# Optimization experiments

Measured on AMD Instinct MI355X. Metric: run time of the kernel, lower is better.

The kernel has to match this reference:

```python
import jax, jax.numpy as jnp
import numpy as np

B, T, H, PRED = 16384, 8, 256, 12


def _cell(x, h, c, Wih, Whh, bih, bhh):
    # PyTorch LSTM gate order: i, f, g, o
    g = x @ Wih.T + h @ Whh.T + bih + bhh
    i, f, gg, o = jnp.split(g, 4, axis=-1)
    c = jax.nn.sigmoid(f) * c + jax.nn.sigmoid(i) * jnp.tanh(gg)
    h = jax.nn.sigmoid(o) * jnp.tanh(c)
    return h, c


def _run_seq(x, layers):
    # stacked LSTM over full sequence, zero initial state; x: [B, T, D]
    b = x.shape[0]
    inp = x
    hs, cs = [], []
    for (Wih, Whh, bih, bhh) in layers:
        h0 = jnp.zeros((b, Whh.shape[1]), x.dtype)

        def step(carry, xt, Wih=Wih, Whh=Whh, bih=bih, bhh=bhh):
            h, c = _cell(xt, carry[0], carry[1], Wih, Whh, bih, bhh)
            return (h, c), h

        (h, c), out = jax.lax.scan(step, (h0, h0), jnp.swapaxes(inp, 0, 1))
        inp = jnp.swapaxes(out, 0, 1)
        hs.append(h)
        cs.append(c)
    return inp, jnp.stack(hs), jnp.stack(cs)


def _step_stack(x, hs, cs, layers):
    # single-timestep pass through stacked LSTM; hs/cs: [L, B, H]
    inp = x
    nh, nc = [], []
    for l, (Wih, Whh, bih, bhh) in enumerate(layers):
        h, c = _cell(inp, hs[l], cs[l], Wih, Whh, bih, bhh)
        inp = h
        nh.append(h)
        nc.append(c)
    return inp, jnp.stack(nh), jnp.stack(nc)


def _forward(x, l1_Wih0, l1_Whh0, l1_bih0, l1_bhh0, l1_Wih1, l1_Whh1, l1_bih1, l1_bhh1,
             l2_Wih0, l2_Whh0, l2_bih0, l2_bhh0, l2_Wih1, l2_Whh1, l2_bih1, l2_bhh1,
             fc1_w, fc1_b, fc2_w, fc2_b):
    L1 = [(l1_Wih0, l1_Whh0, l1_bih0, l1_bhh0), (l1_Wih1, l1_Whh1, l1_bih1, l1_bhh1)]
    L2 = [(l2_Wih0, l2_Whh0, l2_bih0, l2_bhh0), (l2_Wih1, l2_Whh1, l2_bih1, l2_bhh1)]
    out1, h1, c1 = _run_seq(x, L1)           # encode observed track
    _, h2, c2 = _run_seq(out1, L2)
    pos = x[:, -1, :]

    def dec(carry, _):
        pos, h1, c1, h2, c2 = carry
        o1, h1, c1 = _step_stack(pos, h1, c1, L1)
        o2, h2, c2 = _step_stack(o1, h2, c2, L2)
        delta = jax.nn.relu(o2 @ fc1_w.T + fc1_b) @ fc2_w.T + fc2_b
        pos = pos + delta
        return (pos, h1, c1, h2, c2), pos

    _, preds = jax.lax.scan(dec, (pos, h1, c1, h2, c2), None, length=PRED)
    return jnp.swapaxes(preds, 0, 1)  # [B, PRED, 2]


def setup_inputs() -> dict:
    key = jax.random.key(0)
    ks = iter(jax.random.split(key, 32))
    s = 1.0 / np.sqrt(H)  # matches PyTorch LSTM/Linear init scale

    def mk(shape):
        return jax.random.uniform(next(ks), shape, jnp.float32, -s, s)

    d = {"x": jax.random.normal(next(ks), (B, T, 2), jnp.float32)}
    for name, in_dim in [("l1", 2), ("l2", H)]:
        for layer in range(2):
            di = in_dim if layer == 0 else H
            d[f"{name}_Wih{layer}"] = mk((4 * H, di))
            d[f"{name}_Whh{layer}"] = mk((4 * H, H))
            d[f"{name}_bih{layer}"] = mk((4 * H,))
            d[f"{name}_bhh{layer}"] = mk((4 * H,))
    d["fc1_w"] = mk((H, H))
    d["fc1_b"] = mk((H,))
    d["fc2_w"] = mk((2, H))
    d["fc2_b"] = mk((2,))
    return d


def reference(x, l1_Wih0, l1_Whh0, l1_bih0, l1_bhh0, l1_Wih1, l1_Whh1, l1_bih1, l1_bhh1,
              l2_Wih0, l2_Whh0, l2_bih0, l2_bhh0, l2_Wih1, l2_Whh1, l2_bih1, l2_bhh1,
              fc1_w, fc1_b, fc2_w, fc2_b):
    return _forward(x, l1_Wih0, l1_Whh0, l1_bih0, l1_bhh0, l1_Wih1, l1_Whh1, l1_bih1, l1_bhh1,
                    l2_Wih0, l2_Whh0, l2_bih0, l2_bhh0, l2_Wih1, l2_Whh1, l2_bih1, l2_bhh1,
                    fc1_w, fc1_b, fc2_w, fc2_b)
```

## Files before the change

kernel.cpp:

```cpp
#include <hip/hip_runtime.h>
#include <hip/hip_cooperative_groups.h>
#include <stdint.h>

namespace cg = cooperative_groups;

#define Bsz   16384
#define Tseq  8
#define NPRED 12

typedef __attribute__((ext_vector_type(4))) float    f32x4;
typedef _Float16 h16;
typedef __attribute__((ext_vector_type(8))) _Float16 h16x8;

__device__ __forceinline__ float sigf(float x)   { return 1.f / (1.f + __expf(-x)); }
__device__ __forceinline__ float tanh_f(float x) { return 1.f - 2.f / (__expf(2.f * x) + 1.f); }

__device__ __forceinline__ void gload_lds16(const void* g, void* l) {
  __builtin_amdgcn_global_load_lds(
      (const __attribute__((address_space(1))) void*)g,
      (__attribute__((address_space(3))) void*)l, 16, 0, 0);
}

__global__ void mark_r12(float* __restrict__ out) {
  if (blockIdx.x == 0 && threadIdx.x < 64) out[threadIdx.x] = 1000.0f;
}
__global__ void seed_r12(float* __restrict__ pos, const float* __restrict__ x) {
  int b = blockIdx.x * 256 + threadIdx.x;
  pos[2 * b]     = x[(size_t)b * 16 + 14];
  pos[2 * b + 1] = x[(size_t)b * 16 + 15];
}

__global__ void pack_w(h16* __restrict__ dst, const float* __restrict__ W0,
                       const float* __restrict__ W1, int ksplit, int Kw, int Np,
                       int gatePack) {
  int idx = blockIdx.x * 256 + threadIdx.x;
  if (idx >= Np * Kw) return;
  int np = idx / Kw, k = idx - np * Kw;
  int n = np;
  if (gatePack) {
    int jb = np >> 7, wc = (np >> 6) & 1, gi = (np >> 4) & 3, jr = np & 15;
    n = gi * 256 + jb * 32 + wc * 16 + jr;
  }
  float w = (k < ksplit) ? W0[(size_t)n * ksplit + k]
                         : W1[(size_t)n * (Kw - ksplit) + (k - ksplit)];
  int KB = Kw >> 6;
  int jb = np >> 7, r = np & 127, kb = k >> 6;
  uint32_t byte = (uint32_t)(jb * KB + kb) * 16384u + (uint32_t)r * 128u
                + ((2u * (uint32_t)(k & 63)) ^ (uint32_t)((r & 7) << 4));
  *(h16*)((char*)dst + byte) = (h16)w;
}

__global__ void add_bias(float* __restrict__ dst, const float* __restrict__ a,
                         const float* __restrict__ b) {
  int i = blockIdx.x * 256 + threadIdx.x;
  if (i < 1024) dst[i] = a[i] + b[i];
}

__global__ void l0t0_pw(const float* __restrict__ x, const float* __restrict__ wih0,
                        const float* __restrict__ bias, h16* __restrict__ Cst,
                        char* __restrict__ hout) {
  int gid = blockIdx.x * 256 + threadIdx.x;
  int b = gid >> 5, jb = (gid & 31) << 3;
  float x0 = x[(size_t)b * 16], x1 = x[(size_t)b * 16 + 1];
  h16 cc[8]; h16 hh[8];
#pragma unroll
  for (int q = 0; q < 8; ++q) {
    int j = jb + q;
    float vi = bias[j]       + x0 * wih0[2 * j]           + x1 * wih0[2 * j + 1];
    float vg = bias[512 + j] + x0 * wih0[2 * (512 + j)]   + x1 * wih0[2 * (512 + j) + 1];
    float vo = bias[768 + j] + x0 * wih0[2 * (768 + j)]   + x1 * wih0[2 * (768 + j) + 1];
    float cn = sigf(vi) * tanh_f(vg);
    hh[q] = (h16)(sigf(vo) * tanh_f(cn));
    cc[q] = (h16)cn;
  }
  *(h16x8*)(Cst + (size_t)b * 256 + jb) = *(h16x8*)cc;
  *(h16x8*)(hout + (size_t)b * 512 + (((unsigned)jb * 2) ^ (unsigned)((b & 7) << 4))) = *(h16x8*)hh;
}

__device__ __forceinline__ void gemm_core(
    const char* A0, const char* A1, const char* Wp, int KB, int by, int m0,
    char* ldsA, char* ldsB, int tid, f32x4 acc[4][4]) {
  const int wave = tid >> 6, lane = tid & 63;
  const int rowa = tid >> 3;
  const int chb  = (tid & 7) * 16;

#pragma unroll
  for (int m = 0; m < 4; m++)
#pragma unroll
    for (int n = 0; n < 4; n++)
#pragma unroll
      for (int e = 0; e < 4; e++) acc[m][n][e] = 0.f;

  const char* aCur   = A0 + (size_t)(m0 + rowa) * 512 + chb;
  const char* a1Base = A1 + (size_t)(m0 + rowa) * 512 + chb;
  const char* wCur   = Wp + (size_t)by * KB * 16384 + rowa * 128 + chb;

  const int wr = wave >> 1, wc = wave & 1;

  for (int kb = 0; kb < KB; ++kb) {
    if (kb == 4) aCur = a1Base;
#pragma unroll
    for (int it = 0; it < 4; ++it) {
      gload_lds16(aCur + it * 16384, ldsA + it * 4096 + wave * 1024);
      gload_lds16(wCur + it * 4096,  ldsB + it * 4096 + wave * 1024);
    }
    __syncthreads();
#pragma unroll
    for (int kk = 0; kk < 2; ++kk) {
      const int kbyte = kk * 64 + (lane >> 4) * 16;
      h16x8 af[4], bfr[4];
#pragma unroll
      for (int mt = 0; mt < 4; ++mt) {
        int r = wr * 64 + mt * 16 + (lane & 15);
        af[mt] = *(const h16x8*)(ldsA + r * 128 + (kbyte ^ ((r & 7) << 4)));
      }
#pragma unroll
      for (int nt = 0; nt < 4; ++nt) {
        int c = wc * 64 + nt * 16 + (lane & 15);
        bfr[nt] = *(const h16x8*)(ldsB + c * 128 + (kbyte ^ ((c & 7) << 4)));
      }
#pragma unroll
      for (int mt = 0; mt < 4; ++mt)
#pragma unroll
        for (int nt = 0; nt < 4; ++nt)
          acc[mt][nt] = __builtin_amdgcn_mfma_f32_16x16x32_f16(af[mt], bfr[nt], acc[mt][nt], 0, 0, 0);
    }
    __syncthreads();
    aCur += 128;
    wCur += 16384;
  }
}

__device__ __forceinline__ void lstm_epilogue(
    f32x4 acc[4][4], int m0, int n0, int tid, const float* bias,
    const float* wih0, const float* xbase, int xstride, int hasx, int skipc,
    h16* Cst, char* hout) {
  const int wave = tid >> 6, lane = tid & 63;
  const int wr = wave >> 1, wc = wave & 1;
  const int j = (n0 >> 2) + wc * 16 + (lane & 15);
  const float bi = bias[j], bff = bias[256 + j], bg = bias[512 + j], bo = bias[768 + j];
  float wi0 = 0, wi1 = 0, wf0 = 0, wf1 = 0, wg0 = 0, wg1 = 0, wo0 = 0, wo1 = 0;
  if (hasx) {
    wi0 = wih0[2 * j];           wi1 = wih0[2 * j + 1];
    wf0 = wih0[2 * (256 + j)];   wf1 = wih0[2 * (256 + j) + 1];
    wg0 = wih0[2 * (512 + j)];   wg1 = wih0[2 * (512 + j) + 1];
    wo0 = wih0[2 * (768 + j)];   wo1 = wih0[2 * (768 + j) + 1];
  }
#pragma unroll
  for (int mt = 0; mt < 4; ++mt) {
#pragma unroll
    for (int e = 0; e < 4; e++) {
      const int b = m0 + wr * 64 + mt * 16 + (lane >> 4) * 4 + e;
      float vi = acc[mt][0][e] + bi;
      float vf = acc[mt][1][e] + bff;
      float vg = acc[mt][2][e] + bg;
      float vo = acc[mt][3][e] + bo;
      if (hasx) {
        const float x0 = xbase[(size_t)b * xstride];
        const float x1 = xbase[(size_t)b * xstride + 1];
        vi += x0 * wi0 + x1 * wi1;
        vf += x0 * wf0 + x1 * wf1;
        vg += x0 * wg0 + x1 * wg1;
        vo += x0 * wo0 + x1 * wo1;
      }
      const size_t ci = (size_t)b * 256 + j;
      float cn = sigf(vi) * tanh_f(vg);
      if (!skipc) cn += sigf(vf) * (float)Cst[ci];
      float h = sigf(vo) * tanh_f(cn);
      Cst[ci] = (h16)cn;
      *(h16*)(hout + (size_t)b * 512 + (((unsigned)j * 2) ^ (unsigned)((b & 7) << 4))) = (h16)h;
    }
  }
}

__device__ __forceinline__ void head_body(
    const char* A, const char* Wp, const float* b1, const float* w2,
    const float* b2, float* pos, float* out, int s, int blk, int tid, char* lds) {
  const int m0 = blk * 128;
  const int wave = tid >> 6, lane = tid & 63;
  const int wr = wave >> 1, wc = wave & 1;
  const int bl2 = tid >> 1, comp = tid & 1;

  float a = 0.f;
  for (int half = 0; half < 2; ++half) {
    f32x4 acc[4][4];
    gemm_core(A, A, Wp, 4, half, m0, lds, lds + 16384, tid, acc);
    h16* strip = (h16*)lds;
#pragma unroll
    for (int nt = 0; nt < 4; ++nt) {
      const int n = half * 128 + wc * 64 + nt * 16 + (lane & 15);
      const int nl = wc * 64 + nt * 16 + (lane & 15);
      const float bn = b1[n];
#pragma unroll
      for (int mt = 0; mt < 4; ++mt)
#pragma unroll
        for (int e = 0; e < 4; e++) {
          const int bl = wr * 64 + mt * 16 + (lane >> 4) * 4 + e;
          float v = acc[mt][nt][e] + bn;
          strip[bl * 134 + nl] = (h16)(v > 0.f ? v : 0.f);
        }
    }
    __syncthreads();
    const float* wrow = w2 + comp * 256 + half * 128;
#pragma unroll 8
    for (int n = 0; n < 128; ++n)
      a += (float)strip[bl2 * 134 + n] * wrow[n];
    __syncthreads();
  }
  const size_t b = (size_t)(m0 + bl2);
  float p = pos[2 * b + comp] + a + b2[comp];
  pos[2 * b + comp] = p;
  out[b * (NPRED * 2) + s * 2 + comp] = p;
}

struct CellDesc {
  const char* A0; const char* A1; const char* Wp;
  const float* bias; const float* wih0; const float* xbase;
  h16* Cst; char* hout;
  int Kw; int xstride; int hasx; int skipc;
};
struct Fused4 { CellDesc c[4]; };

__global__ __launch_bounds__(256, 4) void cells_diag(Fused4 args) {
  const int cellid = blockIdx.x >> 10;
  const int lid    = blockIdx.x & 1023;
  const CellDesc d = args.c[cellid];

  __shared__ __align__(16) char lds[32768];
  const int tid = threadIdx.x;

  int swz = (lid & 7) * 128 + (lid >> 3);
  const int by = swz & 7, bx = swz >> 3;
  const int m0 = bx * 128, n0 = by * 128;

  f32x4 acc[4][4];
  gemm_core(d.A0, d.A1, d.Wp, d.Kw >> 6, by, m0, lds, lds + 16384, tid, acc);
  lstm_epilogue(acc, m0, n0, tid, d.bias, d.wih0, d.xbase, d.xstride, d.hasx,
                d.skipc, d.Cst, d.hout);
}

struct DecArgs {
  char* hb0[2]; char* hb1[2]; char* hb2[2]; char* hb3[2];
  h16* Cs0; h16* Cs1; h16* Cs2; h16* Cs3;
  const char* wp10; const char* wp0; const char* wp1; const char* wp2; const char* wpf1;
  const float* biasc; const float* wih0;
  const float* fc1_b; const float* fc2_w; const float* fc2_b;
  float* pos; float* out;
};

__global__ __launch_bounds__(256, 4) void decoder_coop(DecArgs a) {
  cg::grid_group grid = cg::this_grid();
  __shared__ __align__(16) char lds[34304];
  const int tid = threadIdx.x;
  const int lid = blockIdx.x;
  int swz = (lid & 7) * 128 + (lid >> 3);
  const int by = swz & 7, bx = swz >> 3;
  const int m0 = bx * 128, n0 = by * 128;

  for (int s = 0; s < NPRED; ++s) {
    const int u = Tseq + s, cur = u & 1, prev = cur ^ 1;
    {
      f32x4 acc[4][4];
      gemm_core(a.hb0[prev], a.hb0[prev], a.wp10, 4, by, m0, lds, lds + 16384, tid, acc);
      lstm_epilogue(acc, m0, n0, tid, a.biasc, a.wih0, a.pos, 2, 1, 0, a.Cs0, a.hb0[cur]);
    }
    __threadfence();  grid.sync();
    {
      f32x4 acc[4][4];
      gemm_core(a.hb0[cur], a.hb1[prev], a.wp0, 8, by, m0, lds, lds + 16384, tid, acc);
      lstm_epilogue(acc, m0, n0, tid, a.biasc + 1024, nullptr, nullptr, 0, 0, 0, a.Cs1, a.hb1[cur]);
    }
    __threadfence();  grid.sync();
    {
      f32x4 acc[4][4];
      gemm_core(a.hb1[cur], a.hb2[prev], a.wp1, 8, by, m0, lds, lds + 16384, tid, acc);
      lstm_epilogue(acc, m0, n0, tid, a.biasc + 2048, nullptr, nullptr, 0, 0, 0, a.Cs2, a.hb2[cur]);
    }
    __threadfence();  grid.sync();
    {
      f32x4 acc[4][4];
      gemm_core(a.hb2[cur], a.hb3[prev], a.wp2, 8, by, m0, lds, lds + 16384, tid, acc);
      lstm_epilogue(acc, m0, n0, tid, a.biasc + 3072, nullptr, nullptr, 0, 0, 0, a.Cs3, a.hb3[cur]);
    }
    __threadfence();  grid.sync();
    if (lid < 128)
      head_body(a.hb3[cur], a.wpf1, a.fc1_b, a.fc2_w, a.fc2_b, a.pos, a.out, s, lid, tid, lds);
    __threadfence();  grid.sync();
  }
}

template <int NSEG, int HASX>
__global__ __launch_bounds__(256, 4) void cell_gemm(
    const char* __restrict__ A0, const char* __restrict__ A1,
    const char* __restrict__ Wp, int Kw,
    const float* __restrict__ bias, const float* __restrict__ wih0,
    const float* __restrict__ xbase, int xstride,
    h16* __restrict__ Cst, char* __restrict__ hout) {
  __shared__ __align__(16) char lds[32768];
  const int tid = threadIdx.x;
  int lid = blockIdx.x;
  int chunkv = gridDim.x >> 3;
  int swz = (lid & 7) * chunkv + (lid >> 3);
  const int by = swz % 8, bx = swz / 8;
  const int m0 = bx * 128, n0 = by * 128;
  f32x4 acc[4][4];
  gemm_core(A0, NSEG == 2 ? A1 : A0, Wp, Kw >> 6, by, m0, lds, lds + 16384, tid, acc);
  lstm_epilogue(acc, m0, n0, tid, bias, wih0, xbase, xstride, HASX, 0, Cst, hout);
}

__global__ __launch_bounds__(256) void fc_head(
    const char* __restrict__ A, const char* __restrict__ Wp,
    const float* __restrict__ b1, const float* __restrict__ w2,
    const float* __restrict__ b2, float* __restrict__ pos,
    float* __restrict__ out, int s) {
  __shared__ __align__(16) char lds[34304];
  head_body(A, Wp, b1, w2, b2, pos, out, s, blockIdx.x, threadIdx.x, lds);
}

extern "C" void kernel_launch(void* const* d_in, const int* in_sizes, int n_in,
                              void* d_out, int out_size, void* d_ws, size_t ws_size,
                              hipStream_t stream) {
  const float* x      = (const float*)d_in[0];
  const float* Wih[4] = {(const float*)d_in[1], (const float*)d_in[5],
                         (const float*)d_in[9], (const float*)d_in[13]};
  const float* Whh[4] = {(const float*)d_in[2], (const float*)d_in[6],
                         (const float*)d_in[10], (const float*)d_in[14]};
  const float* bih[4] = {(const float*)d_in[3], (const float*)d_in[7],
                         (const float*)d_in[11], (const float*)d_in[15]};
  const float* bhh[4] = {(const float*)d_in[4], (const float*)d_in[8],
                         (const float*)d_in[12], (const float*)d_in[16]};
  const float* fc1_w = (const float*)d_in[17];
  const float* fc1_b = (const float*)d_in[18];
  const float* fc2_w = (const float*)d_in[19];
  const float* fc2_b = (const float*)d_in[20];

  char* ws = (char*)d_ws;
  size_t off = 0;
  auto alloc = [&](size_t bytes) -> char* {
    char* p = ws + off;
    off += (bytes + 255) & ~(size_t)255;
    return p;
  };

  h16* Cs[4];
  for (int l = 0; l < 4; l++) Cs[l] = (h16*)alloc((size_t)Bsz * 256 * 2);
  char* h10[2] = {alloc((size_t)Bsz * 512), alloc((size_t)Bsz * 512)};
  char* sl[2]  = {alloc((size_t)Bsz * 512), alloc((size_t)Bsz * 512)};
  char* h20[2] = {alloc((size_t)Bsz * 512), alloc((size_t)Bsz * 512)};
  char* h21[2] = {alloc((size_t)Bsz * 512), alloc((size_t)Bsz * 512)};
  float* pos = (float*)alloc((size_t)Bsz * 2 * 4);
  float* biasc = (float*)alloc(4 * 1024 * 4);
  h16* wp10 = (h16*)alloc((size_t)1024 * 256 * 2);
  h16* wp[3];
  for (int i = 0; i < 3; i++) wp[i] = (h16*)alloc((size_t)1024 * 512 * 2);
  h16* wpf1 = (h16*)alloc((size_t)256 * 256 * 2);

  if (ws_size < off) {
    mark_r12<<<dim3(1), dim3(64), 0, stream>>>((float*)d_out);
    return;
  }

  seed_r12<<<dim3(Bsz / 256), dim3(256), 0, stream>>>(pos, x);

  pack_w<<<dim3((1024 * 256 + 255) / 256), dim3(256), 0, stream>>>(wp10, Whh[0], Whh[0], 256, 256, 1024, 1);
  pack_w<<<dim3((1024 * 512 + 255) / 256), dim3(256), 0, stream>>>(wp[0], Wih[1], Whh[1], 256, 512, 1024, 1);
  pack_w<<<dim3((1024 * 512 + 255) / 256), dim3(256), 0, stream>>>(wp[1], Wih[2], Whh[2], 256, 512, 1024, 1);
  pack_w<<<dim3((1024 * 512 + 255) / 256), dim3(256), 0, stream>>>(wp[2], Wih[3], Whh[3], 256, 512, 1024, 1);
  pack_w<<<dim3((256 * 256 + 255) / 256), dim3(256), 0, stream>>>(wpf1, fc1_w, fc1_w, 256, 256, 256, 0);
  for (int l = 0; l < 4; l++)
    add_bias<<<dim3(4), dim3(256), 0, stream>>>(biasc + l * 1024, bih[l], bhh[l]);

  char* hbuf[4][2] = {{h10[0], h10[1]}, {sl[0], sl[1]}, {h20[0], h20[1]}, {h21[0], h21[1]}};
  const h16* wpl[4] = {wp10, wp[0], wp[1], wp[2]};
  for (int d = 0; d <= 10; d++) {
    if (d == 0) {
      l0t0_pw<<<dim3(2048), dim3(256), 0, stream>>>(x, Wih[0], biasc, Cs[0], hbuf[0][0]);
      continue;
    }
    Fused4 args;
    int nc = 0;
    for (int l = 0; l < 4; l++) {
      int t = d - l;
      if (t < 0 || t >= Tseq) continue;
      CellDesc& cd = args.c[nc++];
      cd.A0 = (l == 0) ? hbuf[0][(t - 1) & 1] : hbuf[l - 1][t & 1];
      cd.A1 = (l > 0 && t > 0) ? hbuf[l][(t - 1) & 1] : cd.A0;
      cd.Wp = (const char*)wpl[l];
      cd.bias = biasc + l * 1024;
      cd.wih0 = (l == 0) ? Wih[0] : nullptr;
      cd.xbase = (l == 0) ? (x + t * 2) : nullptr;
      cd.Cst = Cs[l];
      cd.hout = hbuf[l][t & 1];
      cd.Kw = (l == 0 || t == 0) ? 256 : 512;
      cd.xstride = 16;
      cd.hasx = (l == 0) ? 1 : 0;
      cd.skipc = (t == 0) ? 1 : 0;
    }
    cells_diag<<<dim3(nc * 1024), dim3(256), 0, stream>>>(args);
  }

  int maxb = 0;
  hipError_t oe = hipOccupancyMaxActiveBlocksPerMultiprocessor(&maxb, decoder_coop, 256, 0);
  bool useCoop = (oe == hipSuccess && maxb >= 4);

  if (useCoop) {
    DecArgs da;
    da.hb0[0] = h10[0]; da.hb0[1] = h10[1];
    da.hb1[0] = sl[0];  da.hb1[1] = sl[1];
    da.hb2[0] = h20[0]; da.hb2[1] = h20[1];
    da.hb3[0] = h21[0]; da.hb3[1] = h21[1];
    da.Cs0 = Cs[0]; da.Cs1 = Cs[1]; da.Cs2 = Cs[2]; da.Cs3 = Cs[3];
    da.wp10 = (const char*)wp10; da.wp0 = (const char*)wp[0];
    da.wp1 = (const char*)wp[1]; da.wp2 = (const char*)wp[2];
    da.wpf1 = (const char*)wpf1;
    da.biasc = biasc; da.wih0 = Wih[0];
    da.fc1_b = fc1_b; da.fc2_w = fc2_w; da.fc2_b = fc2_b;
    da.pos = pos; da.out = (float*)d_out;
    void* kargs[] = { &da };
    hipError_t le = hipLaunchCooperativeKernel(decoder_coop, dim3(1024), dim3(256),
                                               kargs, 0, stream);
    if (le == hipSuccess) return;
  }

  for (int s = 0; s < NPRED; s++) {
    int u = Tseq + s, cur = u & 1, prev = cur ^ 1;
    cell_gemm<1, 1><<<dim3(1024), dim3(256), 0, stream>>>(
        h10[prev], h10[prev], (const char*)wp10, 256, biasc, Wih[0], pos, 2, Cs[0], h10[cur]);
    cell_gemm<2, 0><<<dim3(1024), dim3(256), 0, stream>>>(
        h10[cur], sl[prev], (const char*)wp[0], 512, biasc + 1024, nullptr, nullptr, 0, Cs[1], sl[cur]);
    cell_gemm<2, 0><<<dim3(1024), dim3(256), 0, stream>>>(
        sl[cur], h20[prev], (const char*)wp[1], 512, biasc + 2048, nullptr, nullptr, 0, Cs[2], h20[cur]);
    cell_gemm<2, 0><<<dim3(1024), dim3(256), 0, stream>>>(
        h20[cur], h21[prev], (const char*)wp[2], 512, biasc + 3072, nullptr, nullptr, 0, Cs[3], h21[cur]);
    fc_head<<<dim3(128), dim3(256), 0, stream>>>(
        h21[cur], (const char*)wpf1, fc1_b, fc2_w, fc2_b, pos, (float*)d_out, s);
  }
}
```

Baseline: 2.317 ms.

## Widen GEMM tiles to 128x256 with 512-thread blocks for LSTM cells

Changes the GEMM tile from 128x128 with 4 waves to 128x256 with 8 waves, repacks weights into 256-column panels, and halves the grid for the cell, diagonal and cooperative decoder kernels. Each A tile is now loaded once per 256 gate columns instead of once per 128, which cuts redundant activation traffic and halves the number of blocks taking part in each grid sync. The FC head now does its whole 256-wide fc1 in one pass. The cost is more LDS per block (48-66KB) and fewer resident blocks, and the cooperative path now only requires occupancy of 2 blocks per CU.

After: 2.259 ms. 1.03x faster.

```diff
diff --git a/kernel.cpp b/kernel.cpp
--- a/kernel.cpp
+++ b/kernel.cpp
@@ -21,10 +21,10 @@
       (__attribute__((address_space(3))) void*)l, 16, 0, 0);
 }
 
-__global__ void mark_r12(float* __restrict__ out) {
+__global__ void mark_r13(float* __restrict__ out) {
   if (blockIdx.x == 0 && threadIdx.x < 64) out[threadIdx.x] = 1000.0f;
 }
-__global__ void seed_r12(float* __restrict__ pos, const float* __restrict__ x) {
+__global__ void seed_r13(float* __restrict__ pos, const float* __restrict__ x) {
   int b = blockIdx.x * 256 + threadIdx.x;
   pos[2 * b]     = x[(size_t)b * 16 + 14];
   pos[2 * b + 1] = x[(size_t)b * 16 + 15];
@@ -36,16 +36,16 @@
   int idx = blockIdx.x * 256 + threadIdx.x;
   if (idx >= Np * Kw) return;
   int np = idx / Kw, k = idx - np * Kw;
+  int nb = np >> 8, r = np & 255;
   int n = np;
   if (gatePack) {
-    int jb = np >> 7, wc = (np >> 6) & 1, gi = (np >> 4) & 3, jr = np & 15;
-    n = gi * 256 + jb * 32 + wc * 16 + jr;
+    int wcq = r >> 6, gi = (r >> 4) & 3, jr = r & 15;
+    n = gi * 256 + nb * 64 + wcq * 16 + jr;
   }
   float w = (k < ksplit) ? W0[(size_t)n * ksplit + k]
                          : W1[(size_t)n * (Kw - ksplit) + (k - ksplit)];
-  int KB = Kw >> 6;
-  int jb = np >> 7, r = np & 127, kb = k >> 6;
-  uint32_t byte = (uint32_t)(jb * KB + kb) * 16384u + (uint32_t)r * 128u
+  int KB = Kw >> 6, kb = k >> 6;
+  uint32_t byte = (uint32_t)(nb * KB + kb) * 32768u + (uint32_t)r * 128u
                 + ((2u * (uint32_t)(k & 63)) ^ (uint32_t)((r & 7) << 4));
   *(h16*)((char*)dst + byte) = (h16)w;
 }
@@ -79,8 +79,11 @@
 
 __device__ __forceinline__ void gemm_core(
     const char* A0, const char* A1, const char* Wp, int KB, int by, int m0,
-    char* ldsA, char* ldsB, int tid, f32x4 acc[4][4]) {
+    char* lds, int tid, f32x4 acc[4][4]) {
+  char* ldsA = lds;
+  char* ldsB = lds + 16384;
   const int wave = tid >> 6, lane = tid & 63;
+  const int wr = wave >> 2, wc = wave & 3;
   const int rowa = tid >> 3;
   const int chb  = (tid & 7) * 16;
 
@@ -93,17 +96,15 @@
 
   const char* aCur   = A0 + (size_t)(m0 + rowa) * 512 + chb;
   const char* a1Base = A1 + (size_t)(m0 + rowa) * 512 + chb;
-  const char* wCur   = Wp + (size_t)by * KB * 16384 + rowa * 128 + chb;
-
-  const int wr = wave >> 1, wc = wave & 1;
+  const char* wCur   = Wp + (size_t)by * KB * 32768 + (size_t)tid * 16;
 
   for (int kb = 0; kb < KB; ++kb) {
     if (kb == 4) aCur = a1Base;
-#pragma unroll
-    for (int it = 0; it < 4; ++it) {
-      gload_lds16(aCur + it * 16384, ldsA + it * 4096 + wave * 1024);
-      gload_lds16(wCur + it * 4096,  ldsB + it * 4096 + wave * 1024);
-    }
+    gload_lds16(aCur,          ldsA + wave * 1024);
+    gload_lds16(aCur + 32768,  ldsA + 8192 + wave * 1024);
+#pragma unroll
+    for (int it = 0; it < 4; ++it)
+      gload_lds16(wCur + it * 8192, ldsB + it * 8192 + wave * 1024);
     __syncthreads();
 #pragma unroll
     for (int kk = 0; kk < 2; ++kk) {
@@ -127,17 +128,17 @@
     }
     __syncthreads();
     aCur += 128;
-    wCur += 16384;
+    wCur += 32768;
   }
 }
 
 __device__ __forceinline__ void lstm_epilogue(
-    f32x4 acc[4][4], int m0, int n0, int tid, const float* bias,
+    f32x4 acc[4][4], int m0, int by, int tid, const float* bias,
     const float* wih0, const float* xbase, int xstride, int hasx, int skipc,
     h16* Cst, char* hout) {
   const int wave = tid >> 6, lane = tid & 63;
-  const int wr = wave >> 1, wc = wave & 1;
-  const int j = (n0 >> 2) + wc * 16 + (lane & 15);
+  const int wr = wave >> 2, wc = wave & 3;
+  const int j = by * 64 + wc * 16 + (lane & 15);
   const float bi = bias[j], bff = bias[256 + j], bg = bias[512 + j], bo = bias[768 + j];
   float wi0 = 0, wi1 = 0, wf0 = 0, wf1 = 0, wg0 = 0, wg1 = 0, wo0 = 0, wo1 = 0;
   if (hasx) {
@@ -178,39 +179,39 @@
     const float* b2, float* pos, float* out, int s, int blk, int tid, char* lds) {
   const int m0 = blk * 128;
   const int wave = tid >> 6, lane = tid & 63;
-  const int wr = wave >> 1, wc = wave & 1;
-  const int bl2 = tid >> 1, comp = tid & 1;
-
-  float a = 0.f;
-  for (int half = 0; half < 2; ++half) {
-    f32x4 acc[4][4];
-    gemm_core(A, A, Wp, 4, half, m0, lds, lds + 16384, tid, acc);
-    h16* strip = (h16*)lds;
-#pragma unroll
-    for (int nt = 0; nt < 4; ++nt) {
-      const int n = half * 128 + wc * 64 + nt * 16 + (lane & 15);
-      const int nl = wc * 64 + nt * 16 + (lane & 15);
-      const float bn = b1[n];
-#pragma unroll
-      for (int mt = 0; mt < 4; ++mt)
-#pragma unroll
-        for (int e = 0; e < 4; e++) {
-          const int bl = wr * 64 + mt * 16 + (lane >> 4) * 4 + e;
-          float v = acc[mt][nt][e] + bn;
-          strip[bl * 134 + nl] = (h16)(v > 0.f ? v : 0.f);
-        }
-    }
-    __syncthreads();
-    const float* wrow = w2 + comp * 256 + half * 128;
+  const int wr = wave >> 2, wc = wave & 3;
+
+  f32x4 acc[4][4];
+  gemm_core(A, A, Wp, 4, 0, m0, lds, tid, acc);
+
+  h16* strip = (h16*)lds;
+#pragma unroll
+  for (int nt = 0; nt < 4; ++nt) {
+    const int n = wc * 64 + nt * 16 + (lane & 15);
+    const float bn = b1[n];
+#pragma unroll
+    for (int mt = 0; mt < 4; ++mt)
+#pragma unroll
+      for (int e = 0; e < 4; e++) {
+        const int bl = wr * 64 + mt * 16 + (lane >> 4) * 4 + e;
+        float v = acc[mt][nt][e] + bn;
+        strip[bl * 262 + n] = (h16)(v > 0.f ? v : 0.f);
+      }
+  }
+  __syncthreads();
+  if (tid < 256) {
+    const int bl2 = tid >> 1, comp = tid & 1;
+    const float* wrow = w2 + comp * 256;
+    float a = 0.f;
 #pragma unroll 8
-    for (int n = 0; n < 128; ++n)
-      a += (float)strip[bl2 * 134 + n] * wrow[n];
-    __syncthreads();
-  }
-  const size_t b = (size_t)(m0 + bl2);
-  float p = pos[2 * b + comp] + a + b2[comp];
-  pos[2 * b + comp] = p;
-  out[b * (NPRED * 2) + s * 2 + comp] = p;
+    for (int n = 0; n < 256; ++n)
+      a += (float)strip[bl2 * 262 + n] * wrow[n];
+    const size_t b = (size_t)(m0 + bl2);
+    float p = pos[2 * b + comp] + a + b2[comp];
+    pos[2 * b + comp] = p;
+    out[b * (NPRED * 2) + s * 2 + comp] = p;
+  }
+  __syncthreads();
 }
 
 struct CellDesc {
@@ -221,21 +222,21 @@
 };
 struct Fused4 { CellDesc c[4]; };
 
-__global__ __launch_bounds__(256, 4) void cells_diag(Fused4 args) {
-  const int cellid = blockIdx.x >> 10;
-  const int lid    = blockIdx.x & 1023;
+__global__ __launch_bounds__(512, 4) void cells_diag(Fused4 args) {
+  const int cellid = blockIdx.x >> 9;
+  const int lid    = blockIdx.x & 511;
   const CellDesc d = args.c[cellid];
 
-  __shared__ __align__(16) char lds[32768];
+  __shared__ __align__(16) char lds[49152];
   const int tid = threadIdx.x;
 
-  int swz = (lid & 7) * 128 + (lid >> 3);
-  const int by = swz & 7, bx = swz >> 3;
-  const int m0 = bx * 128, n0 = by * 128;
+  int swz = (lid & 7) * 64 + (lid >> 3);
+  const int by = swz & 3, bx = swz >> 2;
+  const int m0 = bx * 128;
 
   f32x4 acc[4][4];
-  gemm_core(d.A0, d.A1, d.Wp, d.Kw >> 6, by, m0, lds, lds + 16384, tid, acc);
-  lstm_epilogue(acc, m0, n0, tid, d.bias, d.wih0, d.xbase, d.xstride, d.hasx,
+  gemm_core(d.A0, d.A1, d.Wp, d.Kw >> 6, by, m0, lds, tid, acc);
+  lstm_epilogue(acc, m0, by, tid, d.bias, d.wih0, d.xbase, d.xstride, d.hasx,
                 d.skipc, d.Cst, d.hout);
 }
 
@@ -248,39 +249,39 @@
   float* pos; float* out;
 };
 
-__global__ __launch_bounds__(256, 4) void decoder_coop(DecArgs a) {
+__global__ __launch_bounds__(512, 4) void decoder_coop(DecArgs a) {
   cg::grid_group grid = cg::this_grid();
-  __shared__ __align__(16) char lds[34304];
+  __shared__ __align__(16) char lds[67072];
   const int tid = threadIdx.x;
   const int lid = blockIdx.x;
-  int swz = (lid & 7) * 128 + (lid >> 3);
-  const int by = swz & 7, bx = swz >> 3;
-  const int m0 = bx * 128, n0 = by * 128;
+  int swz = (lid & 7) * 64 + (lid >> 3);
+  const int by = swz & 3, bx = swz >> 2;
+  const int m0 = bx * 128;
 
   for (int s = 0; s < NPRED; ++s) {
     const int u = Tseq + s, cur = u & 1, prev = cur ^ 1;
     {
       f32x4 acc[4][4];
-      gemm_core(a.hb0[prev], a.hb0[prev], a.wp10, 4, by, m0, lds, lds + 16384, tid, acc);
-      lstm_epilogue(acc, m0, n0, tid, a.biasc, a.wih0, a.pos, 2, 1, 0, a.Cs0, a.hb0[cur]);
+      gemm_core(a.hb0[prev], a.hb0[prev], a.wp10, 4, by, m0, lds, tid, acc);
+      lstm_epilogue(acc, m0, by, tid, a.biasc, a.wih0, a.pos, 2, 1, 0, a.Cs0, a.hb0[cur]);
     }
     __threadfence();  grid.sync();
     {
       f32x4 acc[4][4];
-      gemm_core(a.hb0[cur], a.hb1[prev], a.wp0, 8, by, m0, lds, lds + 16384, tid, acc);
-      lstm_epilogue(acc, m0, n0, tid, a.biasc + 1024, nullptr, nullptr, 0, 0, 0, a.Cs1, a.hb1[cur]);
+      gemm_core(a.hb0[cur], a.hb1[prev], a.wp0, 8, by, m0, lds, tid, acc);
+      lstm_epilogue(acc, m0, by, tid, a.biasc + 1024, nullptr, nullptr, 0, 0, 0, a.Cs1, a.hb1[cur]);
     }
     __threadfence();  grid.sync();
     {
       f32x4 acc[4][4];
-      gemm_core(a.hb1[cur], a.hb2[prev], a.wp1, 8, by, m0, lds, lds + 16384, tid, acc);
-      lstm_epilogue(acc, m0, n0, tid, a.biasc + 2048, nullptr, nullptr, 0, 0, 0, a.Cs2, a.hb2[cur]);
+      gemm_core(a.hb1[cur], a.hb2[prev], a.wp1, 8, by, m0, lds, tid, acc);
+      lstm_epilogue(acc, m0, by, tid, a.biasc + 2048, nullptr, nullptr, 0, 0, 0, a.Cs2, a.hb2[cur]);
     }
     __threadfence();  grid.sync();
     {
       f32x4 acc[4][4];
-      gemm_core(a.hb2[cur], a.hb3[prev], a.wp2, 8, by, m0, lds, lds + 16384, tid, acc);
-      lstm_epilogue(acc, m0, n0, tid, a.biasc + 3072, nullptr, nullptr, 0, 0, 0, a.Cs3, a.hb3[cur]);
+      gemm_core(a.hb2[cur], a.hb3[prev], a.wp2, 8, by, m0, lds, tid, acc);
+      lstm_epilogue(acc, m0, by, tid, a.biasc + 3072, nullptr, nullptr, 0, 0, 0, a.Cs3, a.hb3[cur]);
     }
     __threadfence();  grid.sync();
     if (lid < 128)
@@ -290,30 +291,29 @@
 }
 
 template <int NSEG, int HASX>
-__global__ __launch_bounds__(256, 4) void cell_gemm(
+__global__ __launch_bounds__(512, 4) void cell_gemm(
     const char* __restrict__ A0, const char* __restrict__ A1,
     const char* __restrict__ Wp, int Kw,
     const float* __restrict__ bias, const float* __restrict__ wih0,
     const float* __restrict__ xbase, int xstride,
     h16* __restrict__ Cst, char* __restrict__ hout) {
-  __shared__ __align__(16) char lds[32768];
+  __shared__ __align__(16) char lds[49152];
   const int tid = threadIdx.x;
   int lid = blockIdx.x;
-  int chunkv = gridDim.x >> 3;
-  int swz = (lid & 7) * chunkv + (lid >> 3);
-  const int by = swz % 8, bx = swz / 8;
-  const int m0 = bx * 128, n0 = by * 128;
+  int swz = (lid & 7) * 64 + (lid >> 3);
+  const int by = swz & 3, bx = swz >> 2;
+  const int m0 = bx * 128;
   f32x4 acc[4][4];
-  gemm_core(A0, NSEG == 2 ? A1 : A0, Wp, Kw >> 6, by, m0, lds, lds + 16384, tid, acc);
-  lstm_epilogue(acc, m0, n0, tid, bias, wih0, xbase, xstride, HASX, 0, Cst, hout);
-}
-
-__global__ __launch_bounds__(256) void fc_head(
+  gemm_core(A0, NSEG == 2 ? A1 : A0, Wp, Kw >> 6, by, m0, lds, tid, acc);
+  lstm_epilogue(acc, m0, by, tid, bias, wih0, xbase, xstride, HASX, 0, Cst, hout);
+}
+
+__global__ __launch_bounds__(512) void fc_head(
     const char* __restrict__ A, const char* __restrict__ Wp,
     const float* __restrict__ b1, const float* __restrict__ w2,
     const float* __restrict__ b2, float* __restrict__ pos,
     float* __restrict__ out, int s) {
-  __shared__ __align__(16) char lds[34304];
+  __shared__ __align__(16) char lds[67072];
   head_body(A, Wp, b1, w2, b2, pos, out, s, blockIdx.x, threadIdx.x, lds);
 }
 
@@ -356,11 +356,11 @@
   h16* wpf1 = (h16*)alloc((size_t)256 * 256 * 2);
 
   if (ws_size < off) {
-    mark_r12<<<dim3(1), dim3(64), 0, stream>>>((float*)d_out);
+    mark_r13<<<dim3(1), dim3(64), 0, stream>>>((float*)d_out);
     return;
   }
 
-  seed_r12<<<dim3(Bsz / 256), dim3(256), 0, stream>>>(pos, x);
+  seed_r13<<<dim3(Bsz / 256), dim3(256), 0, stream>>>(pos, x);
 
   pack_w<<<dim3((1024 * 256 + 255) / 256), dim3(256), 0, stream>>>(wp10, Whh[0], Whh[0], 256, 256, 1024, 1);
   pack_w<<<dim3((1024 * 512 + 255) / 256), dim3(256), 0, stream>>>(wp[0], Wih[1], Whh[1], 256, 512, 1024, 1);
@@ -396,12 +396,12 @@
       cd.hasx = (l == 0) ? 1 : 0;
       cd.skipc = (t == 0) ? 1 : 0;
     }
-    cells_diag<<<dim3(nc * 1024), dim3(256), 0, stream>>>(args);
+    cells_diag<<<dim3(nc * 512), dim3(512), 0, stream>>>(args);
   }
 
   int maxb = 0;
-  hipError_t oe = hipOccupancyMaxActiveBlocksPerMultiprocessor(&maxb, decoder_coop, 256, 0);
-  bool useCoop = (oe == hipSuccess && maxb >= 4);
+  hipError_t oe = hipOccupancyMaxActiveBlocksPerMultiprocessor(&maxb, decoder_coop, 512, 0);
+  bool useCoop = (oe == hipSuccess && maxb >= 2);
 
   if (useCoop) {
     DecArgs da;
@@ -417,22 +417,22 @@
     da.fc1_b = fc1_b; da.fc2_w = fc2_w; da.fc2_b = fc2_b;
     da.pos = pos; da.out = (float*)d_out;
     void* kargs[] = { &da };
-    hipError_t le = hipLaunchCooperativeKernel(decoder_coop, dim3(1024), dim3(256),
+    hipError_t le = hipLaunchCooperativeKernel(decoder_coop, dim3(512), dim3(512),
                                                kargs, 0, stream);
     if (le == hipSuccess) return;
   }
 
   for (int s = 0; s < NPRED; s++) {
     int u = Tseq + s, cur = u & 1, prev = cur ^ 1;
-    cell_gemm<1, 1><<<dim3(1024), dim3(256), 0, stream>>>(
+    cell_gemm<1, 1><<<dim3(512), dim3(512), 0, stream>>>(
         h10[prev], h10[prev], (const char*)wp10, 256, biasc, Wih[0], pos, 2, Cs[0], h10[cur]);
-    cell_gemm<2, 0><<<dim3(1024), dim3(256), 0, stream>>>(
+    cell_gemm<2, 0><<<dim3(512), dim3(512), 0, stream>>>(
         h10[cur], sl[prev], (const char*)wp[0], 512, biasc + 1024, nullptr, nullptr, 0, Cs[1], sl[cur]);
-    cell_gemm<2, 0><<<dim3(1024), dim3(256), 0, stream>>>(
+    cell_gemm<2, 0><<<dim3(512), dim3(512), 0, stream>>>(
         sl[cur], h20[prev], (const char*)wp[1], 512, biasc + 2048, nullptr, nullptr, 0, Cs[2], h20[cur]);
-    cell_gemm<2, 0><<<dim3(1024), dim3(256), 0, stream>>>(
+    cell_gemm<2, 0><<<dim3(512), dim3(512), 0, stream>>>(
         h20[cur], h21[prev], (const char*)wp[2], 512, biasc + 3072, nullptr, nullptr, 0, Cs[3], h21[cur]);
-    fc_head<<<dim3(128), dim3(256), 0, stream>>>(
+    fc_head<<<dim3(128), dim3(512), 0, stream>>>(
         h21[cur], (const char*)wpf1, fc1_b, fc2_w, fc2_b, pos, (float*)d_out, s);
   }
 }
```
